# Performance work log

Hardware: AMD Instinct MI355X
Metric: run time of the kernel (lower is better)

The kernel has to match this reference:

```python
import jax, jax.numpy as jnp
import numpy as np

K = 7  # kernel_size


def setup_inputs() -> dict:
    key = jax.random.key(0)
    ks = jax.random.split(key, 7)
    B, C, H, W = 32, 256, 56, 56
    x = jax.random.normal(ks[0], (B, C, H, W), jnp.float32)
    # BatchNorm2d affine params
    bn_gamma = 1.0 + 0.1 * jax.random.normal(ks[1], (C,), jnp.float32)
    bn_beta = 0.1 * jax.random.normal(ks[2], (C,), jnp.float32)
    # Linear(k^2 -> k), torch weight layout (out, in)
    w0 = jax.random.normal(ks[3], (K, K * K), jnp.float32) / np.sqrt(K * K)
    # LayerNorm([C, k]) affine params
    ln_gamma = 1.0 + 0.1 * jax.random.normal(ks[4], (C, K), jnp.float32)
    ln_beta = 0.1 * jax.random.normal(ks[5], (C, K), jnp.float32)
    # Linear(k -> k^2)
    w1 = jax.random.normal(ks[6], (K * K, K), jnp.float32) / np.sqrt(K)
    return dict(x=x, bn_gamma=bn_gamma, bn_beta=bn_beta, w0=w0,
                ln_gamma=ln_gamma, ln_beta=ln_beta, w1=w1)


def reference(x, bn_gamma, bn_beta, w0, ln_gamma, ln_beta, w1):
    B, C, H, W = x.shape
    k = K
    eps = 1e-5
    # AdaptiveAvgPool2d((k,k)); H,W divisible by k -> exact block means
    p = x.reshape(B, C, k, H // k, k, W // k).mean(axis=(3, 5))  # (B,C,k,k)
    # BatchNorm2d (training-mode batch statistics, biased variance)
    mu = p.mean(axis=(0, 2, 3), keepdims=True)
    var = p.var(axis=(0, 2, 3), keepdims=True)
    p = (p - mu) * jax.lax.rsqrt(var + eps)
    p = p * bn_gamma[None, :, None, None] + bn_beta[None, :, None, None]
    # b c kh kw -> b c (kh kw), then Linear(k^2 -> k)
    v = p.reshape(B, C, k * k) @ w0.T  # (B,C,k)
    # LayerNorm over the (C,k) normalized shape
    m = v.mean(axis=(1, 2), keepdims=True)
    s = v.var(axis=(1, 2), keepdims=True)
    v = (v - m) * jax.lax.rsqrt(s + eps) * ln_gamma[None] + ln_beta[None]
    v = jax.nn.sigmoid(v)
    v = v @ w1.T  # (B,C,k^2)
    kern = v.reshape(B * C, 1, k, k)  # per-sample, per-channel depthwise kernels
    # F.conv2d(groups=B*C, padding='same', stride=1); odd k -> 'SAME' matches torch
    out = jax.lax.conv_general_dilated(
        x.reshape(1, B * C, H, W), kern,
        window_strides=(1, 1), padding='SAME',
        feature_group_count=B * C,
        dimension_numbers=('NCHW', 'OIHW', 'NCHW'))
    return out.reshape(B, C, H, W)
```

## Files before the change

### kernel.cpp

```cpp
#include <hip/hip_runtime.h>
#include <math.h>

#define BATCH 32
#define CH    256
#define HH    56
#define WW    56
#define HW    3136
#define KS    7
#define KK    49
#define NIMG  8192
#define PITCH 64
#define PROWS 62

__global__ __launch_bounds__(256) void pool_kernel(const float* __restrict__ x,
                                                   float* __restrict__ p) {
    __shared__ float tile[HW];
    const int img = blockIdx.x;
    const float* xi = x + (size_t)img * HW;
    for (int i = threadIdx.x; i < HW; i += 256) tile[i] = xi[i];
    __syncthreads();
    if (threadIdx.x < KK) {
        const int pr = threadIdx.x / KS, pc = threadIdx.x % KS;
        float s = 0.f;
        #pragma unroll
        for (int r = 0; r < 8; ++r) {
            const int base = (pr * 8 + r) * WW + pc * 8;
            #pragma unroll
            for (int c = 0; c < 8; ++c) s += tile[base + c];
        }
        p[(size_t)img * KK + threadIdx.x] = s * (1.0f / 64.0f);
    }
}

__global__ __launch_bounds__(256) void bnstats_kernel(const float* __restrict__ p,
                                                      const float* __restrict__ gamma,
                                                      const float* __restrict__ beta,
                                                      float* __restrict__ scale,
                                                      float* __restrict__ shift) {
    const int c = blockIdx.x;
    float s = 0.f, s2 = 0.f;
    for (int t = threadIdx.x; t < BATCH * KK; t += 256) {
        const int b = t / KK, i = t - b * KK;
        const float v = p[((size_t)b * CH + c) * KK + i];
        s += v; s2 += v * v;
    }
    #pragma unroll
    for (int o = 32; o >= 1; o >>= 1) {
        s  += __shfl_down(s, o, 64);
        s2 += __shfl_down(s2, o, 64);
    }
    __shared__ float r1[4], r2[4];
    const int w = threadIdx.x >> 6;
    if ((threadIdx.x & 63) == 0) { r1[w] = s; r2[w] = s2; }
    __syncthreads();
    if (threadIdx.x == 0) {
        const float S  = r1[0] + r1[1] + r1[2] + r1[3];
        const float S2 = r2[0] + r2[1] + r2[2] + r2[3];
        const float inv = 1.0f / (float)(BATCH * KK);
        const float mu  = S * inv;
        const float var = S2 * inv - mu * mu;
        const float rstd = rsqrtf(var + 1e-5f);
        const float sc = gamma[c] * rstd;
        scale[c] = sc;
        shift[c] = beta[c] - mu * sc;
    }
}

__global__ __launch_bounds__(256) void mid_kernel(const float* __restrict__ p,
                                                  const float* __restrict__ scale,
                                                  const float* __restrict__ shift,
                                                  const float* __restrict__ w0,
                                                  const float* __restrict__ lng,
                                                  const float* __restrict__ lnb,
                                                  const float* __restrict__ w1,
                                                  float* __restrict__ ker) {
    const int b = blockIdx.x, c = threadIdx.x;
    __shared__ float s_w0[KS * KK], s_w1[KK * KS];
    __shared__ float r1[4], r2[4];
    for (int i = threadIdx.x; i < KS * KK; i += 256) { s_w0[i] = w0[i]; s_w1[i] = w1[i]; }
    __syncthreads();
    float pn[KK];
    const float* pp = p + ((size_t)b * CH + c) * KK;
    const float sc = scale[c], sh = shift[c];
    #pragma unroll
    for (int i = 0; i < KK; ++i) pn[i] = pp[i] * sc + sh;
    float v[KS];
    float ls = 0.f, ls2 = 0.f;
    #pragma unroll
    for (int j = 0; j < KS; ++j) {
        float a = 0.f;
        #pragma unroll
        for (int i = 0; i < KK; ++i) a += pn[i] * s_w0[j * KK + i];
        v[j] = a; ls += a; ls2 += a * a;
    }
    #pragma unroll
    for (int o = 32; o >= 1; o >>= 1) {
        ls  += __shfl_down(ls, o, 64);
        ls2 += __shfl_down(ls2, o, 64);
    }
    const int w = threadIdx.x >> 6;
    if ((threadIdx.x & 63) == 0) { r1[w] = ls; r2[w] = ls2; }
    __syncthreads();
    const float S  = r1[0] + r1[1] + r1[2] + r1[3];
    const float S2 = r2[0] + r2[1] + r2[2] + r2[3];
    const float inv = 1.0f / (float)(CH * KS);
    const float m   = S * inv;
    const float var = S2 * inv - m * m;
    const float rs  = rsqrtf(var + 1e-5f);
    float sg[KS];
    #pragma unroll
    for (int j = 0; j < KS; ++j) {
        const float vn = (v[j] - m) * rs * lng[c * KS + j] + lnb[c * KS + j];
        sg[j] = 1.0f / (1.0f + expf(-vn));
    }
    float* ko = ker + ((size_t)b * CH + c) * KK;
    #pragma unroll
    for (int i = 0; i < KK; ++i) {
        float a = 0.f;
        #pragma unroll
        for (int j = 0; j < KS; ++j) a += sg[j] * s_w1[i * KS + j];
        ko[i] = a;
    }
}

__global__ __launch_bounds__(448) void conv_kernel(const float* __restrict__ x,
                                                   const float* __restrict__ ker,
                                                   float* __restrict__ out) {
    __shared__ float pad[PROWS * PITCH];
    __shared__ float kf[KK];
    const int img = blockIdx.x;
    const int t = threadIdx.x;
    const float* xi = x + (size_t)img * HW;
    if (t < KK) kf[t] = ker[(size_t)img * KK + t];
    for (int i = t; i < PROWS * PITCH; i += 448) {
        const int pr = i >> 6, pc = i & 63;
        const int r = pr - 3, c = pc - 3;
        float v = 0.f;
        if (r >= 0 && r < HH && c >= 0 && c < WW) v = xi[r * WW + c];
        pad[i] = v;
    }
    __syncthreads();
    const int col = t % 56;
    const int r0  = (t / 56) * 7;
    float acc[7] = {0.f, 0.f, 0.f, 0.f, 0.f, 0.f, 0.f};
    #pragma unroll
    for (int kw = 0; kw < 7; ++kw) {
        float wv[13];
        #pragma unroll
        for (int rr = 0; rr < 13; ++rr) wv[rr] = pad[(r0 + rr) * PITCH + col + kw];
        #pragma unroll
        for (int kr = 0; kr < 7; ++kr) {
            const float kv = kf[kr * 7 + kw];
            #pragma unroll
            for (int rr = 0; rr < 7; ++rr) acc[rr] += wv[rr + kr] * kv;
        }
    }
    float* oi = out + (size_t)img * HW;
    #pragma unroll
    for (int rr = 0; rr < 7; ++rr) oi[(r0 + rr) * WW + col] = acc[rr];
}

extern "C" void kernel_launch(void* const* d_in, const int* in_sizes, int n_in,
                              void* d_out, int out_size, void* d_ws, size_t ws_size,
                              hipStream_t stream) {
    const float* x   = (const float*)d_in[0];
    const float* bng = (const float*)d_in[1];
    const float* bnb = (const float*)d_in[2];
    const float* w0  = (const float*)d_in[3];
    const float* lng = (const float*)d_in[4];
    const float* lnb = (const float*)d_in[5];
    const float* w1  = (const float*)d_in[6];
    float* out = (float*)d_out;

    float* ws    = (float*)d_ws;
    float* p     = ws;
    float* scale = p + (size_t)NIMG * KK;
    float* shift = scale + CH;
    float* kern  = shift + CH;

    hipLaunchKernelGGL(pool_kernel,    dim3(NIMG),  dim3(256), 0, stream, x, p);
    hipLaunchKernelGGL(bnstats_kernel, dim3(CH),    dim3(256), 0, stream, p, bng, bnb, scale, shift);
    hipLaunchKernelGGL(mid_kernel,     dim3(BATCH), dim3(256), 0, stream, p, scale, shift,
                       w0, lng, lnb, w1, kern);
    hipLaunchKernelGGL(conv_kernel,    dim3(NIMG),  dim3(448), 0, stream, x, kern, out);
}
```

Measured before the change: 263.4 us.

## Fuse BN stats into pooling, vectorize pool loads, register-tile the depthwise conv

```diff
diff --git a/kernel.cpp b/kernel.cpp
--- a/kernel.cpp
+++ b/kernel.cpp
@@ -9,66 +9,52 @@
 #define KS    7
 #define KK    49
 #define NIMG  8192
-#define PITCH 64
-#define PROWS 62
+#define CPITCH 72
+#define CROWS  62
+#define CPIMG  (CROWS*CPITCH)
+#define CIPB   2
 
 __global__ __launch_bounds__(256) void pool_kernel(const float* __restrict__ x,
-                                                   float* __restrict__ p) {
-    __shared__ float tile[HW];
-    const int img = blockIdx.x;
-    const float* xi = x + (size_t)img * HW;
-    for (int i = threadIdx.x; i < HW; i += 256) tile[i] = xi[i];
-    __syncthreads();
-    if (threadIdx.x < KK) {
-        const int pr = threadIdx.x / KS, pc = threadIdx.x % KS;
-        float s = 0.f;
+                                                   float* __restrict__ p,
+                                                   float2* __restrict__ ss) {
+    const int t  = threadIdx.x;
+    const int im = t >> 7, tl = t & 127;
+    const int img = blockIdx.x * 2 + im;
+    const bool active = tl < 98;
+    float s = 0.f;
+    if (active) {
+        const int cq = tl % 14, pr = tl / 14;
+        const float4* xr = (const float4*)(x + (size_t)img * HW);
         #pragma unroll
         for (int r = 0; r < 8; ++r) {
-            const int base = (pr * 8 + r) * WW + pc * 8;
-            #pragma unroll
-            for (int c = 0; c < 8; ++c) s += tile[base + c];
+            const float4 v = xr[(pr * 8 + r) * 14 + cq];
+            s += (v.x + v.y) + (v.z + v.w);
         }
-        p[(size_t)img * KK + threadIdx.x] = s * (1.0f / 64.0f);
-    }
-}
-
-__global__ __launch_bounds__(256) void bnstats_kernel(const float* __restrict__ p,
-                                                      const float* __restrict__ gamma,
-                                                      const float* __restrict__ beta,
-                                                      float* __restrict__ scale,
-                                                      float* __restrict__ shift) {
-    const int c = blockIdx.x;
-    float s = 0.f, s2 = 0.f;
-    for (int t = threadIdx.x; t < BATCH * KK; t += 256) {
-        const int b = t / KK, i = t - b * KK;
-        const float v = p[((size_t)b * CH + c) * KK + i];
-        s += v; s2 += v * v;
-    }
+    }
+    const float cellv = (s + __shfl_xor(s, 1, 64)) * (1.0f / 64.0f);
+    float v = 0.f;
+    if (active && !(tl & 1)) {
+        const int cq = tl % 14, pr = tl / 14;
+        p[(size_t)img * KK + pr * KS + (cq >> 1)] = cellv;
+        v = cellv;
+    }
+    float v2 = v * v;
     #pragma unroll
     for (int o = 32; o >= 1; o >>= 1) {
-        s  += __shfl_down(s, o, 64);
-        s2 += __shfl_down(s2, o, 64);
-    }
-    __shared__ float r1[4], r2[4];
-    const int w = threadIdx.x >> 6;
-    if ((threadIdx.x & 63) == 0) { r1[w] = s; r2[w] = s2; }
-    __syncthreads();
-    if (threadIdx.x == 0) {
-        const float S  = r1[0] + r1[1] + r1[2] + r1[3];
-        const float S2 = r2[0] + r2[1] + r2[2] + r2[3];
-        const float inv = 1.0f / (float)(BATCH * KK);
-        const float mu  = S * inv;
-        const float var = S2 * inv - mu * mu;
-        const float rstd = rsqrtf(var + 1e-5f);
-        const float sc = gamma[c] * rstd;
-        scale[c] = sc;
-        shift[c] = beta[c] - mu * sc;
-    }
+        v  += __shfl_down(v,  o, 64);
+        v2 += __shfl_down(v2, o, 64);
+    }
+    __shared__ float ps1[4], ps2[4];
+    if ((t & 63) == 0) { ps1[t >> 6] = v; ps2[t >> 6] = v2; }
+    __syncthreads();
+    if (t == 0)  ss[img]     = make_float2(ps1[0] + ps1[1], ps2[0] + ps2[1]);
+    if (t == 64) ss[img + 1] = make_float2(ps1[2] + ps1[3], ps2[2] + ps2[3]);
 }
 
 __global__ __launch_bounds__(256) void mid_kernel(const float* __restrict__ p,
-                                                  const float* __restrict__ scale,
-                                                  const float* __restrict__ shift,
+                                                  const float2* __restrict__ ss,
+                                                  const float* __restrict__ bng,
+                                                  const float* __restrict__ bnb,
                                                   const float* __restrict__ w0,
                                                   const float* __restrict__ lng,
                                                   const float* __restrict__ lnb,
@@ -77,13 +63,26 @@
     const int b = blockIdx.x, c = threadIdx.x;
     __shared__ float s_w0[KS * KK], s_w1[KK * KS];
     __shared__ float r1[4], r2[4];
-    for (int i = threadIdx.x; i < KS * KK; i += 256) { s_w0[i] = w0[i]; s_w1[i] = w1[i]; }
+    for (int i = c; i < KS * KK; i += 256) { s_w0[i] = w0[i]; s_w1[i] = w1[i]; }
+    float S = 0.f, S2 = 0.f;
+    #pragma unroll 4
+    for (int bb = 0; bb < BATCH; ++bb) {
+        const float2 t2 = ss[(size_t)bb * CH + c];
+        S += t2.x; S2 += t2.y;
+    }
+    {
+        const float inv  = 1.0f / (float)(BATCH * KK);
+        const float mu   = S * inv;
+        const float var  = S2 * inv - mu * mu;
+        const float rstd = rsqrtf(var + 1e-5f);
+        S  = bng[c] * rstd;
+        S2 = bnb[c] - mu * S;
+    }
     __syncthreads();
     float pn[KK];
     const float* pp = p + ((size_t)b * CH + c) * KK;
-    const float sc = scale[c], sh = shift[c];
-    #pragma unroll
-    for (int i = 0; i < KK; ++i) pn[i] = pp[i] * sc + sh;
+    #pragma unroll
+    for (int i = 0; i < KK; ++i) pn[i] = pp[i] * S + S2;
     float v[KS];
     float ls = 0.f, ls2 = 0.f;
     #pragma unroll
@@ -101,11 +100,11 @@
     const int w = threadIdx.x >> 6;
     if ((threadIdx.x & 63) == 0) { r1[w] = ls; r2[w] = ls2; }
     __syncthreads();
-    const float S  = r1[0] + r1[1] + r1[2] + r1[3];
-    const float S2 = r2[0] + r2[1] + r2[2] + r2[3];
+    const float Sv  = r1[0] + r1[1] + r1[2] + r1[3];
+    const float Sv2 = r2[0] + r2[1] + r2[2] + r2[3];
     const float inv = 1.0f / (float)(CH * KS);
-    const float m   = S * inv;
-    const float var = S2 * inv - m * m;
+    const float m   = Sv * inv;
+    const float var = Sv2 * inv - m * m;
     const float rs  = rsqrtf(var + 1e-5f);
     float sg[KS];
     #pragma unroll
@@ -123,41 +122,68 @@
     }
 }
 
-__global__ __launch_bounds__(448) void conv_kernel(const float* __restrict__ x,
+__global__ __launch_bounds__(256) void conv_kernel(const float* __restrict__ x,
                                                    const float* __restrict__ ker,
                                                    float* __restrict__ out) {
-    __shared__ float pad[PROWS * PITCH];
-    __shared__ float kf[KK];
-    const int img = blockIdx.x;
-    const int t = threadIdx.x;
-    const float* xi = x + (size_t)img * HW;
-    if (t < KK) kf[t] = ker[(size_t)img * KK + t];
-    for (int i = t; i < PROWS * PITCH; i += 448) {
-        const int pr = i >> 6, pc = i & 63;
-        const int r = pr - 3, c = pc - 3;
-        float v = 0.f;
-        if (r >= 0 && r < HH && c >= 0 && c < WW) v = xi[r * WW + c];
-        pad[i] = v;
-    }
-    __syncthreads();
-    const int col = t % 56;
-    const int r0  = (t / 56) * 7;
-    float acc[7] = {0.f, 0.f, 0.f, 0.f, 0.f, 0.f, 0.f};
-    #pragma unroll
-    for (int kw = 0; kw < 7; ++kw) {
-        float wv[13];
-        #pragma unroll
-        for (int rr = 0; rr < 13; ++rr) wv[rr] = pad[(r0 + rr) * PITCH + col + kw];
-        #pragma unroll
-        for (int kr = 0; kr < 7; ++kr) {
-            const float kv = kf[kr * 7 + kw];
+    __shared__ __align__(16) float pad[CIPB * CPIMG];
+    __shared__ float kfl[CIPB * KK];
+    const int t    = threadIdx.x;
+    const int img0 = blockIdx.x * CIPB;
+    if (t < CIPB * KK) kfl[t] = ker[(size_t)img0 * KK + t];
+    float4* pz = (float4*)pad;
+    for (int j = t; j < CIPB * CPIMG / 4; j += 256)
+        pz[j] = make_float4(0.f, 0.f, 0.f, 0.f);
+    __syncthreads();
+    for (int jj = t; jj < CIPB * 784; jj += 256) {
+        const int imS = (jj >= 784) ? 1 : 0;
+        const int j   = jj - imS * 784;
+        const int r   = j / 14, c4 = j - r * 14;
+        const float4 v = *(const float4*)(x + (size_t)(img0 + imS) * HW + r * WW + c4 * 4);
+        float* d = pad + imS * CPIMG + (r + 3) * CPITCH + c4 * 4 + 3;
+        d[0] = v.x; d[1] = v.y; d[2] = v.z; d[3] = v.w;
+    }
+    __syncthreads();
+    const int im = t >> 7, tl = t & 127;
+    const int q = tl & 15, st = tl >> 4;
+    const int oc0 = q * 4, orow0 = st * 7;
+    float kv[KK];
+    #pragma unroll
+    for (int i = 0; i < KK; ++i)
+        kv[i] = __int_as_float(__builtin_amdgcn_readfirstlane(__float_as_int(kfl[im * KK + i])));
+    const float* pb = pad + im * CPIMG + orow0 * CPITCH + oc0;
+    float acc[KS][4];
+    #pragma unroll
+    for (int a = 0; a < KS; ++a)
+        #pragma unroll
+        for (int d = 0; d < 4; ++d) acc[a][d] = 0.f;
+    #pragma unroll
+    for (int ri = 0; ri < 13; ++ri) {
+        const float4 A  = *(const float4*)(pb + ri * CPITCH);
+        const float4 Bv = *(const float4*)(pb + ri * CPITCH + 4);
+        const float4 Cv = *(const float4*)(pb + ri * CPITCH + 8);
+        const float w[12] = {A.x, A.y, A.z, A.w, Bv.x, Bv.y, Bv.z, Bv.w,
+                             Cv.x, Cv.y, Cv.z, Cv.w};
+        #pragma unroll
+        for (int kr = 0; kr < KS; ++kr) {
+            const int orow = ri - kr;
+            if (orow < 0 || orow > 6) continue;
             #pragma unroll
-            for (int rr = 0; rr < 7; ++rr) acc[rr] += wv[rr + kr] * kv;
+            for (int kw = 0; kw < KS; ++kw) {
+                const float kvv = kv[kr * KS + kw];
+                acc[orow][0] += w[kw    ] * kvv;
+                acc[orow][1] += w[kw + 1] * kvv;
+                acc[orow][2] += w[kw + 2] * kvv;
+                acc[orow][3] += w[kw + 3] * kvv;
+            }
         }
     }
-    float* oi = out + (size_t)img * HW;
-    #pragma unroll
-    for (int rr = 0; rr < 7; ++rr) oi[(r0 + rr) * WW + col] = acc[rr];
+    if (q < 14) {
+        float* oi = out + (size_t)(img0 + im) * HW;
+        #pragma unroll
+        for (int rr = 0; rr < KS; ++rr)
+            *(float4*)&oi[(orow0 + rr) * WW + oc0] =
+                make_float4(acc[rr][0], acc[rr][1], acc[rr][2], acc[rr][3]);
+    }
 }
 
 extern "C" void kernel_launch(void* const* d_in, const int* in_sizes, int n_in,
@@ -172,15 +198,13 @@
     const float* w1  = (const float*)d_in[6];
     float* out = (float*)d_out;
 
-    float* ws    = (float*)d_ws;
-    float* p     = ws;
-    float* scale = p + (size_t)NIMG * KK;
-    float* shift = scale + CH;
-    float* kern  = shift + CH;
-
-    hipLaunchKernelGGL(pool_kernel,    dim3(NIMG),  dim3(256), 0, stream, x, p);
-    hipLaunchKernelGGL(bnstats_kernel, dim3(CH),    dim3(256), 0, stream, p, bng, bnb, scale, shift);
-    hipLaunchKernelGGL(mid_kernel,     dim3(BATCH), dim3(256), 0, stream, p, scale, shift,
-                       w0, lng, lnb, w1, kern);
-    hipLaunchKernelGGL(conv_kernel,    dim3(NIMG),  dim3(448), 0, stream, x, kern, out);
-}
+    float* ws   = (float*)d_ws;
+    float* p    = ws;
+    float* kern = p + (size_t)NIMG * KK;
+    float2* ss  = (float2*)d_out;
+
+    hipLaunchKernelGGL(pool_kernel, dim3(NIMG / 2),    dim3(256), 0, stream, x, p, ss);
+    hipLaunchKernelGGL(mid_kernel,  dim3(BATCH),       dim3(256), 0, stream, p, ss,
+                       bng, bnb, w0, lng, lnb, w1, kern);
+    hipLaunchKernelGGL(conv_kernel, dim3(NIMG / CIPB), dim3(256), 0, stream, x, kern, out);
+}
```

Measured after the change: 249.6 us. 1.06x faster.
